# Kernel optimization log

Measured on AMD Instinct MI355X. Metric: run time of the kernel, lower is better.

## Reference

```python
import jax, jax.numpy as jnp
import numpy as np

DIM = 1024
NUM_HEADS = 16
NUM_KV_HEADS = 4
HEAD_DIM = DIM // NUM_HEADS  # 64
QK_GAIN = 1.5
ROPE_BASE = 10000.0


def _rms_norm(x, eps):
    # F.rms_norm with no weight: x / sqrt(mean(x^2) + eps)
    ms = jnp.mean(jnp.square(x), axis=-1, keepdims=True)
    return x * jax.lax.rsqrt(ms + eps)


def _rope_tables(seqlen, dim, dtype):
    inv_freq = 1.0 / (ROPE_BASE ** (jnp.arange(0, dim, 2, dtype=jnp.float32) / dim))
    freqs = jnp.outer(jnp.arange(seqlen, dtype=jnp.float32), inv_freq)  # [N, D/2]
    emb = jnp.concatenate([freqs, freqs], axis=-1)  # [N, D]
    return jnp.cos(emb).astype(dtype), jnp.sin(emb).astype(dtype)


def _apply_rope(x, cos, sin):
    # x: [B, N, H, D]; cos/sin: [N, D] broadcast over batch and heads
    half = x.shape[-1] // 2
    rot = jnp.concatenate([-x[..., half:], x[..., :half]], axis=-1)
    return x * cos[None, :, None, :] + rot * sin[None, :, None, :]


def setup_inputs() -> dict:
    key = jax.random.key(0)
    ks = jax.random.split(key, 5)
    B, N, C = 4, 2048, DIM
    s = 0.02
    return {
        "x": jax.random.normal(ks[0], (B, N, C), dtype=jnp.float32),
        "wq": jax.random.normal(ks[1], (C, C), dtype=jnp.float32) * s,
        "wk": jax.random.normal(ks[2], (C, NUM_KV_HEADS * HEAD_DIM), dtype=jnp.float32) * s,
        "wv": jax.random.normal(ks[3], (C, NUM_KV_HEADS * HEAD_DIM), dtype=jnp.float32) * s,
        "wo": jax.random.normal(ks[4], (C, C), dtype=jnp.float32) * s,
    }


def reference(x, wq, wk, wv, wo) -> jnp.ndarray:
    B, N, C = x.shape
    H, Hkv, D = NUM_HEADS, NUM_KV_HEADS, HEAD_DIM
    eps = jnp.finfo(x.dtype).eps

    q = (x @ wq).reshape(B, N, H, D)
    k = (x @ wk).reshape(B, N, Hkv, D)
    v = (x @ wv).reshape(B, N, Hkv, D)

    q = _rms_norm(q, eps)
    k = _rms_norm(k, eps)

    cos, sin = _rope_tables(N, D, q.dtype)
    q = _apply_rope(q, cos, sin) * QK_GAIN
    k = _apply_rope(k, cos, sin)

    # GQA head expansion (repeat_interleave along head dim)
    g = H // Hkv
    k = jnp.repeat(k, g, axis=2)  # [B, N, H, D]
    v = jnp.repeat(v, g, axis=2)

    # causal SDPA, scale = 1/sqrt(D)
    scores = jnp.einsum("bqhd,bkhd->bhqk", q, k) / jnp.sqrt(jnp.asarray(D, q.dtype))
    causal = jnp.tril(jnp.ones((N, N), dtype=bool))
    scores = jnp.where(causal[None, None], scores, jnp.finfo(scores.dtype).min)
    probs = jax.nn.softmax(scores, axis=-1)
    y = jnp.einsum("bhqk,bkhd->bqhd", probs, v).reshape(B, N, C)
    return y @ wo
```

## Files before the change

### kernel.cpp

```cpp
#include <hip/hip_runtime.h>

typedef __bf16 bf16;
typedef __bf16 bf16x8 __attribute__((ext_vector_type(8)));
typedef __bf16 bf16x4 __attribute__((ext_vector_type(4)));
typedef float f32x4 __attribute__((ext_vector_type(4)));

#define B_ 4
#define N_ 2048
#define C_ 1024
#define H_ 16
#define HKV_ 4
#define D_ 64

#define QSCALE 0.2705053201666806f
#define NEGINF (-1.0e30f)
#define ROPE_C (-0.41524101186092029f)

__global__ __launch_bounds__(256) void prep_qkv(const float* __restrict__ wq,
                                                const float* __restrict__ wk,
                                                const float* __restrict__ wv,
                                                bf16* __restrict__ wT) {
  __shared__ __align__(16) bf16 lds[64 * 72];
  int bx = blockIdx.x;
  const float* w;
  int ncols, tk, tn, nbase;
  if (bx < 256) {
    w = wq; ncols = 1024; tk = bx >> 4; tn = bx & 15; nbase = 0;
  } else if (bx < 320) {
    int t = bx - 256;
    w = wk; ncols = 256; tk = t >> 2; tn = t & 3; nbase = 1024;
  } else {
    int t = bx - 320;
    w = wv; ncols = 256; tk = t >> 2; tn = t & 3; nbase = 1280;
  }
  int tid = threadIdx.x;
#pragma unroll
  for (int i = 0; i < 4; ++i) {
    int c = tid + i * 256;
    int kr = c >> 4, n4 = (c & 15) * 4;
    f32x4 v = *(const f32x4*)(w + (size_t)(tk * 64 + kr) * ncols + tn * 64 + n4);
    bf16x4 b;
#pragma unroll
    for (int j = 0; j < 4; ++j) b[j] = (bf16)v[j];
    *(bf16x4*)(lds + kr * 72 + n4) = b;
  }
  __syncthreads();
#pragma unroll
  for (int i = 0; i < 2; ++i) {
    int c = tid + i * 256;
    int n = c >> 3, koff = (c & 7) * 8;
    bf16x8 tv;
#pragma unroll
    for (int j = 0; j < 8; ++j) tv[j] = lds[(koff + j) * 72 + n];
    *(bf16x8*)(wT + (size_t)(nbase + tn * 64 + n) * 1024 + tk * 64 + koff) = tv;
  }
}

__global__ __launch_bounds__(256) void prep_wo(const float* __restrict__ w,
                                               bf16* __restrict__ wT) {
  __shared__ __align__(16) bf16 lds[64 * 72];
  int tk = blockIdx.x >> 4, tn = blockIdx.x & 15;
  int tid = threadIdx.x;
#pragma unroll
  for (int i = 0; i < 4; ++i) {
    int c = tid + i * 256;
    int kr = c >> 4, n4 = (c & 15) * 4;
    f32x4 v = *(const f32x4*)(w + (size_t)(tk * 64 + kr) * 1024 + tn * 64 + n4);
    bf16x4 b;
#pragma unroll
    for (int j = 0; j < 4; ++j) b[j] = (bf16)v[j];
    *(bf16x4*)(lds + kr * 72 + n4) = b;
  }
  __syncthreads();
#pragma unroll
  for (int i = 0; i < 2; ++i) {
    int c = tid + i * 256;
    int n = c >> 3, koff = (c & 7) * 8;
    bf16x8 tv;
#pragma unroll
    for (int j = 0; j < 8; ++j) tv[j] = lds[(koff + j) * 72 + n];
    *(bf16x8*)(wT + (size_t)(tn * 64 + n) * 1024 + tk * 64 + koff) = tv;
  }
}

__global__ __launch_bounds__(256) void gemm_qkv(const float* __restrict__ x,
                                                const bf16* __restrict__ wT,
                                                bf16* __restrict__ qb,
                                                bf16* __restrict__ kvK,
                                                bf16* __restrict__ vt) {
  __shared__ __align__(16) bf16 As[128 * 72];
  __shared__ __align__(16) bf16 Bs[128 * 72];
  int by = blockIdx.y;
  int n0 = by * 128;
  int m0 = blockIdx.x * 128;
  int tid = threadIdx.x;
  int wave = tid >> 6, lane = tid & 63;
  int quad = lane >> 4, lr = lane & 15;
  int wr = (wave >> 1) * 64, wc = (wave & 1) * 64;
  int arow = tid >> 4, aoff = (tid & 15) * 4;
  int brow = tid >> 3, boff = (tid & 7) * 8;

  f32x4 acc[4][4];
  const f32x4 z = {0.f, 0.f, 0.f, 0.f};
#pragma unroll
  for (int i = 0; i < 4; ++i)
#pragma unroll
    for (int j = 0; j < 4; ++j) acc[i][j] = z;

  f32x4 sa[8];
  bf16x8 sb[4];
#pragma unroll
  for (int i = 0; i < 8; ++i)
    sa[i] = *(const f32x4*)(x + (size_t)(m0 + arow + i * 16) * 1024 + aoff);
#pragma unroll
  for (int i = 0; i < 4; ++i)
    sb[i] = *(const bf16x8*)(wT + (size_t)(n0 + brow + i * 32) * 1024 + boff);
#pragma unroll
  for (int i = 0; i < 8; ++i) {
    bf16x4 a16;
#pragma unroll
    for (int j = 0; j < 4; ++j) a16[j] = (bf16)sa[i][j];
    *(bf16x4*)(As + (arow + i * 16) * 72 + aoff) = a16;
  }
#pragma unroll
  for (int i = 0; i < 4; ++i) *(bf16x8*)(Bs + (brow + i * 32) * 72 + boff) = sb[i];
  asm volatile("s_waitcnt lgkmcnt(0)" ::: "memory");
  __builtin_amdgcn_s_barrier();
  __builtin_amdgcn_sched_barrier(0);

  for (int k0 = 0; k0 < 1024; k0 += 64) {
    bool pf = (k0 + 64 < 1024);
    if (pf) {
#pragma unroll
      for (int i = 0; i < 8; ++i)
        sa[i] = *(const f32x4*)(x + (size_t)(m0 + arow + i * 16) * 1024 + k0 + 64 + aoff);
#pragma unroll
      for (int i = 0; i < 4; ++i)
        sb[i] = *(const bf16x8*)(wT + (size_t)(n0 + brow + i * 32) * 1024 + k0 + 64 + boff);
    }
#pragma unroll
    for (int kx = 0; kx < 2; ++kx) {
      bf16x8 af[4], bfr[4];
#pragma unroll
      for (int t = 0; t < 4; ++t) {
        af[t] = *(const bf16x8*)(As + (wr + t * 16 + lr) * 72 + kx * 32 + quad * 8);
        bfr[t] = *(const bf16x8*)(Bs + (wc + t * 16 + lr) * 72 + kx * 32 + quad * 8);
      }
      __builtin_amdgcn_s_setprio(1);
#pragma unroll
      for (int rt = 0; rt < 4; ++rt)
#pragma unroll
        for (int ct = 0; ct < 4; ++ct)
          acc[rt][ct] = __builtin_amdgcn_mfma_f32_16x16x32_bf16(af[rt], bfr[ct],
                                                                acc[rt][ct], 0, 0, 0);
      __builtin_amdgcn_s_setprio(0);
    }
    __builtin_amdgcn_s_barrier();
    __builtin_amdgcn_sched_barrier(0);
    if (pf) {
#pragma unroll
      for (int i = 0; i < 8; ++i) {
        bf16x4 a16;
#pragma unroll
        for (int j = 0; j < 4; ++j) a16[j] = (bf16)sa[i][j];
        *(bf16x4*)(As + (arow + i * 16) * 72 + aoff) = a16;
      }
#pragma unroll
      for (int i = 0; i < 4; ++i) *(bf16x8*)(Bs + (brow + i * 32) * 72 + boff) = sb[i];
      asm volatile("s_waitcnt lgkmcnt(0)" ::: "memory");
    }
    __builtin_amdgcn_s_barrier();
    __builtin_amdgcn_sched_barrier(0);
  }

  if (by < 10) {
    bf16* Out;
    int ostride, ocol0;
    float oscale;
    if (by < 8) {
      Out = qb; ostride = 1024; ocol0 = by * 128; oscale = QSCALE;
    } else {
      Out = kvK; ostride = 256; ocol0 = (by - 8) * 128; oscale = 1.0f;
    }
    float if0 = exp2f(ROPE_C * (float)lr);
    float if1 = exp2f(ROPE_C * (float)(16 + lr));
#pragma unroll
    for (int rt = 0; rt < 4; ++rt) {
#pragma unroll
      for (int r = 0; r < 4; ++r) {
        float ss = 0.f;
#pragma unroll
        for (int ct = 0; ct < 4; ++ct) ss += acc[rt][ct][r] * acc[rt][ct][r];
        ss += __shfl_xor(ss, 1);
        ss += __shfl_xor(ss, 2);
        ss += __shfl_xor(ss, 4);
        ss += __shfl_xor(ss, 8);
        float rn = rsqrtf(ss * (1.0f / 64.0f) + 1.1920929e-07f);
        int row = m0 + wr + rt * 16 + quad * 4 + r;
        float fn = (float)(row & (N_ - 1));
        float sv0, cv0, sv1, cv1;
        __sincosf(fn * if0, &sv0, &cv0);
        __sincosf(fn * if1, &sv1, &cv1);
#pragma unroll
        for (int ct = 0; ct < 4; ++ct) {
          float xn = acc[rt][ct][r] * rn;
          float xp = acc[rt][ct ^ 2][r] * rn;
          float rot = (ct < 2) ? -xp : xp;
          float sv = (ct & 1) ? sv1 : sv0;
          float cv = (ct & 1) ? cv1 : cv0;
          int col = ocol0 + wc + ct * 16 + lr;
          Out[(size_t)row * ostride + col] = (bf16)((xn * cv + rot * sv) * oscale);
        }
      }
    }
  } else {
    int b = m0 >> 11;
    int tokb = (m0 & (N_ - 1)) + wr;
    int hv = (by - 10) * 2 + (wc >> 6);
#pragma unroll
    for (int rt = 0; rt < 4; ++rt)
#pragma unroll
      for (int ct = 0; ct < 4; ++ct) {
        bf16x4 ov;
#pragma unroll
        for (int r = 0; r < 4; ++r) ov[r] = (bf16)acc[rt][ct][r];
        int d = ct * 16 + lr;
        int tok = tokb + rt * 16 + quad * 4;
        *(bf16x4*)(vt + ((size_t)((b * 4 + hv) * 64 + d)) * N_ + tok) = ov;
      }
  }
}

__global__ __launch_bounds__(256) void gemm_out(const bf16* __restrict__ A,
                                                const bf16* __restrict__ Bt,
                                                float* __restrict__ C) {
  __shared__ __align__(16) bf16 As[128 * 72];
  __shared__ __align__(16) bf16 Bs[128 * 72];
  int m0 = blockIdx.x * 128, n0 = blockIdx.y * 128;
  int tid = threadIdx.x;
  int wave = tid >> 6, lane = tid & 63;
  int quad = lane >> 4, lr = lane & 15;
  int wr = (wave >> 1) * 64, wc = (wave & 1) * 64;
  int brow = tid >> 3, boff = (tid & 7) * 8;

  f32x4 acc[4][4];
  const f32x4 z = {0.f, 0.f, 0.f, 0.f};
#pragma unroll
  for (int i = 0; i < 4; ++i)
#pragma unroll
    for (int j = 0; j < 4; ++j) acc[i][j] = z;

  bf16x8 sa[4], sb[4];
#pragma unroll
  for (int i = 0; i < 4; ++i) {
    sa[i] = *(const bf16x8*)(A + (size_t)(m0 + brow + i * 32) * 1024 + boff);
    sb[i] = *(const bf16x8*)(Bt + (size_t)(n0 + brow + i * 32) * 1024 + boff);
  }
#pragma unroll
  for (int i = 0; i < 4; ++i) {
    *(bf16x8*)(As + (brow + i * 32) * 72 + boff) = sa[i];
    *(bf16x8*)(Bs + (brow + i * 32) * 72 + boff) = sb[i];
  }
  asm volatile("s_waitcnt lgkmcnt(0)" ::: "memory");
  __builtin_amdgcn_s_barrier();
  __builtin_amdgcn_sched_barrier(0);

  for (int k0 = 0; k0 < 1024; k0 += 64) {
    bool pf = (k0 + 64 < 1024);
    if (pf) {
#pragma unroll
      for (int i = 0; i < 4; ++i) {
        sa[i] = *(const bf16x8*)(A + (size_t)(m0 + brow + i * 32) * 1024 + k0 + 64 + boff);
        sb[i] = *(const bf16x8*)(Bt + (size_t)(n0 + brow + i * 32) * 1024 + k0 + 64 + boff);
      }
    }
#pragma unroll
    for (int kx = 0; kx < 2; ++kx) {
      bf16x8 af[4], bfr[4];
#pragma unroll
      for (int t = 0; t < 4; ++t) {
        af[t] = *(const bf16x8*)(As + (wr + t * 16 + lr) * 72 + kx * 32 + quad * 8);
        bfr[t] = *(const bf16x8*)(Bs + (wc + t * 16 + lr) * 72 + kx * 32 + quad * 8);
      }
      __builtin_amdgcn_s_setprio(1);
#pragma unroll
      for (int rt = 0; rt < 4; ++rt)
#pragma unroll
        for (int ct = 0; ct < 4; ++ct)
          acc[rt][ct] = __builtin_amdgcn_mfma_f32_16x16x32_bf16(af[rt], bfr[ct],
                                                                acc[rt][ct], 0, 0, 0);
      __builtin_amdgcn_s_setprio(0);
    }
    __builtin_amdgcn_s_barrier();
    __builtin_amdgcn_sched_barrier(0);
    if (pf) {
#pragma unroll
      for (int i = 0; i < 4; ++i) {
        *(bf16x8*)(As + (brow + i * 32) * 72 + boff) = sa[i];
        *(bf16x8*)(Bs + (brow + i * 32) * 72 + boff) = sb[i];
      }
      asm volatile("s_waitcnt lgkmcnt(0)" ::: "memory");
    }
    __builtin_amdgcn_s_barrier();
    __builtin_amdgcn_sched_barrier(0);
  }
#pragma unroll
  for (int rt = 0; rt < 4; ++rt)
#pragma unroll
    for (int ct = 0; ct < 4; ++ct)
#pragma unroll
      for (int r = 0; r < 4; ++r) {
        int row = m0 + wr + rt * 16 + quad * 4 + r;
        int col = n0 + wc + ct * 16 + lr;
        C[(size_t)row * 1024 + col] = acc[rt][ct][r];
      }
}

__global__ __launch_bounds__(256) void attn(bf16* __restrict__ q,
                                            const bf16* __restrict__ kv,
                                            const bf16* __restrict__ vt) {
  __shared__ __align__(16) bf16 Ks[2][64 * 64];
  __shared__ __align__(16) bf16 Vs[2][64 * 64];
  __shared__ __align__(16) bf16 Ps[64 * 64];
  int bid = blockIdx.x;
  int orig = (bid & 7) * 128 + (bid >> 3);
  int grp = orig >> 6;
  int inner = orig & 63;
  int b = grp >> 2, hkv = grp & 3;
  int h = hkv * 4 + (inner & 3);
  int p = inner >> 2;
  int tid = threadIdx.x;
  int wave = tid >> 6, lane = tid & 63;
  int quad = lane >> 4, lr = lane & 15;
  int srow = tid >> 3, soff = (tid & 7) * 8;
  int su = ((tid & 7) ^ (srow & 7)) * 8;
  int e7 = lr & 7;
  const f32x4 z = {0.f, 0.f, 0.f, 0.f};

#pragma unroll 1
  for (int s = 0; s < 2; ++s) {
    int j = s ? (31 - p) : p;
    __syncthreads();
    int qrow0 = j * 64 + wave * 16;
    int nkt = j + 1;

    bf16x8 qf[2];
#pragma unroll
    for (int kx = 0; kx < 2; ++kx)
      qf[kx] = *(const bf16x8*)(
          q + ((size_t)(b * N_ + qrow0 + lr) * H_ + h) * D_ + kx * 32 + quad * 8);

    f32x4 acc[4];
    float l_i = 0.f;
#pragma unroll
    for (int dt = 0; dt < 4; ++dt) acc[dt] = z;

    const bf16* kp = kv + (size_t)(b * N_ + srow) * 256 + hkv * 64 + soff;
    const bf16* vp = vt + ((size_t)(b * HKV_ + hkv) * 64 + srow) * N_ + soff;

    bf16x8 sk0, sk1, sv0, sv1;
    sk0 = *(const bf16x8*)(kp);
    sk1 = *(const bf16x8*)(kp + 32 * 256);
    sv0 = *(const bf16x8*)(vp);
    sv1 = *(const bf16x8*)(vp + 32 * N_);
    *(bf16x8*)(Ks[0] + srow * 64 + su) = sk0;
    *(bf16x8*)(Ks[0] + (srow + 32) * 64 + su) = sk1;
    *(bf16x8*)(Vs[0] + srow * 64 + su) = sv0;
    *(bf16x8*)(Vs[0] + (srow + 32) * 64 + su) = sv1;
    if (nkt > 1) {
      kp += 64 * 256;
      vp += 64;
      sk0 = *(const bf16x8*)(kp);
      sk1 = *(const bf16x8*)(kp + 32 * 256);
      sv0 = *(const bf16x8*)(vp);
      sv1 = *(const bf16x8*)(vp + 32 * N_);
    }
    asm volatile("s_waitcnt lgkmcnt(0)" ::: "memory");
    __builtin_amdgcn_s_barrier();
    __builtin_amdgcn_sched_barrier(0);

    int cur = 0;
    for (int kt = 0; kt < nkt; ++kt) {
      const bf16* Kc = Ks[cur];
      const bf16* Vc = Vs[cur];
      f32x4 st[4];
#pragma unroll
      for (int ct = 0; ct < 4; ++ct) st[ct] = z;
#pragma unroll
      for (int kx = 0; kx < 2; ++kx) {
        bf16x8 kf[4];
#pragma unroll
        for (int ct = 0; ct < 4; ++ct)
          kf[ct] = *(const bf16x8*)(Kc + (ct * 16 + lr) * 64 + (((kx * 4 + quad) ^ e7) * 8));
        __builtin_amdgcn_s_setprio(1);
#pragma unroll
        for (int ct = 0; ct < 4; ++ct)
          st[ct] = __builtin_amdgcn_mfma_f32_16x16x32_bf16(kf[ct], qf[kx], st[ct], 0, 0, 0);
        __builtin_amdgcn_s_setprio(0);
      }
      if (kt == j) {
        int qrow = qrow0 + lr;
#pragma unroll
        for (int ct = 0; ct < 4; ++ct)
#pragma unroll
          for (int r = 0; r < 4; ++r) {
            int key = kt * 64 + ct * 16 + quad * 4 + r;
            if (key > qrow) st[ct][r] = NEGINF;
          }
      }
      float rs = 0.f;
#pragma unroll
      for (int ct = 0; ct < 4; ++ct)
#pragma unroll
        for (int r = 0; r < 4; ++r) {
          float pv = exp2f(st[ct][r]);
          st[ct][r] = pv;
          rs += pv;
        }
      rs += __shfl_xor(rs, 16);
      rs += __shfl_xor(rs, 32);
      l_i += rs;
#pragma unroll
      for (int ct = 0; ct < 4; ++ct) {
        bf16x4 pk;
#pragma unroll
        for (int r = 0; r < 4; ++r) pk[r] = (bf16)st[ct][r];
        int pu = (((ct * 2) + (quad >> 1)) ^ e7) * 8 + (quad & 1) * 4;
        *(bf16x4*)(Ps + (wave * 16 + lr) * 64 + pu) = pk;
      }
      asm volatile("s_waitcnt lgkmcnt(0)" ::: "memory");
#pragma unroll
      for (int kx = 0; kx < 2; ++kx) {
        bf16x8 vf[4], pfr;
#pragma unroll
        for (int dt = 0; dt < 4; ++dt)
          vf[dt] = *(const bf16x8*)(Vc + (dt * 16 + lr) * 64 + (((kx * 4 + quad) ^ e7) * 8));
        pfr = *(const bf16x8*)(Ps + (wave * 16 + lr) * 64 + (((kx * 4 + quad) ^ e7) * 8));
        __builtin_amdgcn_s_setprio(1);
#pragma unroll
        for (int dt = 0; dt < 4; ++dt)
          acc[dt] = __builtin_amdgcn_mfma_f32_16x16x32_bf16(vf[dt], pfr, acc[dt], 0, 0, 0);
        __builtin_amdgcn_s_setprio(0);
      }

      bool pf = (kt + 1 < nkt);
      if (pf) {
        bf16* Kn = Ks[cur ^ 1];
        bf16* Vn = Vs[cur ^ 1];
        *(bf16x8*)(Kn + srow * 64 + su) = sk0;
        *(bf16x8*)(Kn + (srow + 32) * 64 + su) = sk1;
        *(bf16x8*)(Vn + srow * 64 + su) = sv0;
        *(bf16x8*)(Vn + (srow + 32) * 64 + su) = sv1;
        if (kt + 2 < nkt) {
          kp += 64 * 256;
          vp += 64;
          sk0 = *(const bf16x8*)(kp);
          sk1 = *(const bf16x8*)(kp + 32 * 256);
          sv0 = *(const bf16x8*)(vp);
          sv1 = *(const bf16x8*)(vp + 32 * N_);
        }
        asm volatile("s_waitcnt lgkmcnt(0)" ::: "memory");
      }
      __builtin_amdgcn_s_barrier();
      __builtin_amdgcn_sched_barrier(0);
      cur ^= 1;
    }

    float inv = 1.0f / l_i;
    int qrow = qrow0 + lr;
#pragma unroll
    for (int dt = 0; dt < 4; ++dt) {
      bf16x4 ov;
#pragma unroll
      for (int r = 0; r < 4; ++r) ov[r] = (bf16)(acc[dt][r] * inv);
      *(bf16x4*)(q + ((size_t)(b * N_ + qrow) * H_ + h) * D_ + dt * 16 + quad * 4) = ov;
    }
  }
}

extern "C" void kernel_launch(void* const* d_in, const int* in_sizes, int n_in,
                              void* d_out, int out_size, void* d_ws, size_t ws_size,
                              hipStream_t stream) {
  const float* x = (const float*)d_in[0];
  const float* wq = (const float*)d_in[1];
  const float* wk = (const float*)d_in[2];
  const float* wv = (const float*)d_in[3];
  const float* wo = (const float*)d_in[4];
  float* out = (float*)d_out;
  char* ws = (char*)d_ws;
  bf16* q = (bf16*)(ws);
  bf16* kvK = (bf16*)(ws + 16777216);
  bf16* vt = (bf16*)(ws + 20971520);
  bf16* wqkvT = (bf16*)(ws + 25165824);
  bf16* woT = (bf16*)(ws + 25165824);

  prep_qkv<<<dim3(384), 256, 0, stream>>>(wq, wk, wv, wqkvT);
  gemm_qkv<<<dim3(64, 12), 256, 0, stream>>>(x, wqkvT, q, kvK, vt);
  attn<<<dim3(1024), 256, 0, stream>>>(q, kvK, vt);
  prep_wo<<<dim3(256), 256, 0, stream>>>(wo, woT);
  gemm_out<<<dim3(64, 8), 256, 0, stream>>>(q, woT, out);
}
```

Before: 234.3 us.

## Stage GEMM tiles via direct global-to-LDS loads with XOR swizzle, pre-convert x

Adds a prep kernel that converts x to bf16, writing it into the output buffer as scratch. Both GEMMs now load tiles with global_load_lds straight into an XOR-swizzled, unpadded LDS layout instead of staging through registers. This removes the register prefetch and the manual LDS stores, but it also drops the overlap of next-tile loads with the MFMAs, so each k-step now waits at a barrier for its own loads. The extra conversion pass adds a read of x and a write of its bf16 copy.

```diff
diff --git a/kernel.cpp b/kernel.cpp
--- a/kernel.cpp
+++ b/kernel.cpp
@@ -15,6 +15,26 @@
 #define QSCALE 0.2705053201666806f
 #define NEGINF (-1.0e30f)
 #define ROPE_C (-0.41524101186092029f)
+
+__device__ __forceinline__ void glds16(const bf16* g, bf16* l) {
+  __builtin_amdgcn_global_load_lds(
+      (const __attribute__((address_space(1))) void*)g,
+      (__attribute__((address_space(3))) void*)l, 16, 0, 0);
+}
+
+__global__ __launch_bounds__(256) void prep_x(const float* __restrict__ x,
+                                              bf16* __restrict__ xb) {
+  size_t i = ((size_t)blockIdx.x * 256 + threadIdx.x) * 8;
+  f32x4 a = *(const f32x4*)(x + i);
+  f32x4 b = *(const f32x4*)(x + i + 4);
+  bf16x8 o;
+#pragma unroll
+  for (int j = 0; j < 4; ++j) {
+    o[j] = (bf16)a[j];
+    o[4 + j] = (bf16)b[j];
+  }
+  *(bf16x8*)(xb + i) = o;
+}
 
 __global__ __launch_bounds__(256) void prep_qkv(const float* __restrict__ wq,
                                                 const float* __restrict__ wk,
@@ -83,22 +103,25 @@
   }
 }
 
-__global__ __launch_bounds__(256) void gemm_qkv(const float* __restrict__ x,
+__global__ __launch_bounds__(256) void gemm_qkv(const bf16* __restrict__ xb,
                                                 const bf16* __restrict__ wT,
                                                 bf16* __restrict__ qb,
                                                 bf16* __restrict__ kvK,
                                                 bf16* __restrict__ vt) {
-  __shared__ __align__(16) bf16 As[128 * 72];
-  __shared__ __align__(16) bf16 Bs[128 * 72];
+  __shared__ __align__(16) bf16 As[128 * 64];
+  __shared__ __align__(16) bf16 Bs[128 * 64];
   int by = blockIdx.y;
   int n0 = by * 128;
   int m0 = blockIdx.x * 128;
   int tid = threadIdx.x;
-  int wave = tid >> 6, lane = tid & 63;
+  int lane = tid & 63;
+  int w8 = __builtin_amdgcn_readfirstlane(tid >> 6) * 8;
+  int wave = tid >> 6;
   int quad = lane >> 4, lr = lane & 15;
   int wr = (wave >> 1) * 64, wc = (wave & 1) * 64;
-  int arow = tid >> 4, aoff = (tid & 15) * 4;
-  int brow = tid >> 3, boff = (tid & 7) * 8;
+  int e7 = lr & 7;
+  int srow = w8 + (lane >> 3);
+  int sunit = (lane & 7) ^ (lane >> 3);
 
   f32x4 acc[4][4];
   const f32x4 z = {0.f, 0.f, 0.f, 0.f};
@@ -107,44 +130,23 @@
 #pragma unroll
     for (int j = 0; j < 4; ++j) acc[i][j] = z;
 
-  f32x4 sa[8];
-  bf16x8 sb[4];
-#pragma unroll
-  for (int i = 0; i < 8; ++i)
-    sa[i] = *(const f32x4*)(x + (size_t)(m0 + arow + i * 16) * 1024 + aoff);
-#pragma unroll
-  for (int i = 0; i < 4; ++i)
-    sb[i] = *(const bf16x8*)(wT + (size_t)(n0 + brow + i * 32) * 1024 + boff);
-#pragma unroll
-  for (int i = 0; i < 8; ++i) {
-    bf16x4 a16;
-#pragma unroll
-    for (int j = 0; j < 4; ++j) a16[j] = (bf16)sa[i][j];
-    *(bf16x4*)(As + (arow + i * 16) * 72 + aoff) = a16;
-  }
-#pragma unroll
-  for (int i = 0; i < 4; ++i) *(bf16x8*)(Bs + (brow + i * 32) * 72 + boff) = sb[i];
-  asm volatile("s_waitcnt lgkmcnt(0)" ::: "memory");
-  __builtin_amdgcn_s_barrier();
-  __builtin_amdgcn_sched_barrier(0);
-
   for (int k0 = 0; k0 < 1024; k0 += 64) {
-    bool pf = (k0 + 64 < 1024);
-    if (pf) {
-#pragma unroll
-      for (int i = 0; i < 8; ++i)
-        sa[i] = *(const f32x4*)(x + (size_t)(m0 + arow + i * 16) * 1024 + k0 + 64 + aoff);
-#pragma unroll
-      for (int i = 0; i < 4; ++i)
-        sb[i] = *(const bf16x8*)(wT + (size_t)(n0 + brow + i * 32) * 1024 + k0 + 64 + boff);
-    }
+    __syncthreads();
+#pragma unroll
+    for (int i = 0; i < 4; ++i) {
+      glds16(xb + (size_t)(m0 + i * 32 + srow) * 1024 + k0 + sunit * 8,
+             As + (i * 32 + w8) * 64);
+      glds16(wT + (size_t)(n0 + i * 32 + srow) * 1024 + k0 + sunit * 8,
+             Bs + (i * 32 + w8) * 64);
+    }
+    __syncthreads();
 #pragma unroll
     for (int kx = 0; kx < 2; ++kx) {
       bf16x8 af[4], bfr[4];
 #pragma unroll
       for (int t = 0; t < 4; ++t) {
-        af[t] = *(const bf16x8*)(As + (wr + t * 16 + lr) * 72 + kx * 32 + quad * 8);
-        bfr[t] = *(const bf16x8*)(Bs + (wc + t * 16 + lr) * 72 + kx * 32 + quad * 8);
+        af[t] = *(const bf16x8*)(As + (wr + t * 16 + lr) * 64 + (((kx * 4 + quad) ^ e7) * 8));
+        bfr[t] = *(const bf16x8*)(Bs + (wc + t * 16 + lr) * 64 + (((kx * 4 + quad) ^ e7) * 8));
       }
       __builtin_amdgcn_s_setprio(1);
 #pragma unroll
@@ -155,22 +157,6 @@
                                                                 acc[rt][ct], 0, 0, 0);
       __builtin_amdgcn_s_setprio(0);
     }
-    __builtin_amdgcn_s_barrier();
-    __builtin_amdgcn_sched_barrier(0);
-    if (pf) {
-#pragma unroll
-      for (int i = 0; i < 8; ++i) {
-        bf16x4 a16;
-#pragma unroll
-        for (int j = 0; j < 4; ++j) a16[j] = (bf16)sa[i][j];
-        *(bf16x4*)(As + (arow + i * 16) * 72 + aoff) = a16;
-      }
-#pragma unroll
-      for (int i = 0; i < 4; ++i) *(bf16x8*)(Bs + (brow + i * 32) * 72 + boff) = sb[i];
-      asm volatile("s_waitcnt lgkmcnt(0)" ::: "memory");
-    }
-    __builtin_amdgcn_s_barrier();
-    __builtin_amdgcn_sched_barrier(0);
   }
 
   if (by < 10) {
@@ -234,14 +220,18 @@
 __global__ __launch_bounds__(256) void gemm_out(const bf16* __restrict__ A,
                                                 const bf16* __restrict__ Bt,
                                                 float* __restrict__ C) {
-  __shared__ __align__(16) bf16 As[128 * 72];
-  __shared__ __align__(16) bf16 Bs[128 * 72];
+  __shared__ __align__(16) bf16 As[128 * 64];
+  __shared__ __align__(16) bf16 Bs[128 * 64];
   int m0 = blockIdx.x * 128, n0 = blockIdx.y * 128;
   int tid = threadIdx.x;
-  int wave = tid >> 6, lane = tid & 63;
+  int lane = tid & 63;
+  int w8 = __builtin_amdgcn_readfirstlane(tid >> 6) * 8;
+  int wave = tid >> 6;
   int quad = lane >> 4, lr = lane & 15;
   int wr = (wave >> 1) * 64, wc = (wave & 1) * 64;
-  int brow = tid >> 3, boff = (tid & 7) * 8;
+  int e7 = lr & 7;
+  int srow = w8 + (lane >> 3);
+  int sunit = (lane & 7) ^ (lane >> 3);
 
   f32x4 acc[4][4];
   const f32x4 z = {0.f, 0.f, 0.f, 0.f};
@@ -250,37 +240,23 @@
 #pragma unroll
     for (int j = 0; j < 4; ++j) acc[i][j] = z;
 
-  bf16x8 sa[4], sb[4];
-#pragma unroll
-  for (int i = 0; i < 4; ++i) {
-    sa[i] = *(const bf16x8*)(A + (size_t)(m0 + brow + i * 32) * 1024 + boff);
-    sb[i] = *(const bf16x8*)(Bt + (size_t)(n0 + brow + i * 32) * 1024 + boff);
-  }
-#pragma unroll
-  for (int i = 0; i < 4; ++i) {
-    *(bf16x8*)(As + (brow + i * 32) * 72 + boff) = sa[i];
-    *(bf16x8*)(Bs + (brow + i * 32) * 72 + boff) = sb[i];
-  }
-  asm volatile("s_waitcnt lgkmcnt(0)" ::: "memory");
-  __builtin_amdgcn_s_barrier();
-  __builtin_amdgcn_sched_barrier(0);
-
   for (int k0 = 0; k0 < 1024; k0 += 64) {
-    bool pf = (k0 + 64 < 1024);
-    if (pf) {
-#pragma unroll
-      for (int i = 0; i < 4; ++i) {
-        sa[i] = *(const bf16x8*)(A + (size_t)(m0 + brow + i * 32) * 1024 + k0 + 64 + boff);
-        sb[i] = *(const bf16x8*)(Bt + (size_t)(n0 + brow + i * 32) * 1024 + k0 + 64 + boff);
-      }
-    }
+    __syncthreads();
+#pragma unroll
+    for (int i = 0; i < 4; ++i) {
+      glds16(A + (size_t)(m0 + i * 32 + srow) * 1024 + k0 + sunit * 8,
+             As + (i * 32 + w8) * 64);
+      glds16(Bt + (size_t)(n0 + i * 32 + srow) * 1024 + k0 + sunit * 8,
+             Bs + (i * 32 + w8) * 64);
+    }
+    __syncthreads();
 #pragma unroll
     for (int kx = 0; kx < 2; ++kx) {
       bf16x8 af[4], bfr[4];
 #pragma unroll
       for (int t = 0; t < 4; ++t) {
-        af[t] = *(const bf16x8*)(As + (wr + t * 16 + lr) * 72 + kx * 32 + quad * 8);
-        bfr[t] = *(const bf16x8*)(Bs + (wc + t * 16 + lr) * 72 + kx * 32 + quad * 8);
+        af[t] = *(const bf16x8*)(As + (wr + t * 16 + lr) * 64 + (((kx * 4 + quad) ^ e7) * 8));
+        bfr[t] = *(const bf16x8*)(Bs + (wc + t * 16 + lr) * 64 + (((kx * 4 + quad) ^ e7) * 8));
       }
       __builtin_amdgcn_s_setprio(1);
 #pragma unroll
@@ -291,18 +267,6 @@
                                                                 acc[rt][ct], 0, 0, 0);
       __builtin_amdgcn_s_setprio(0);
     }
-    __builtin_amdgcn_s_barrier();
-    __builtin_amdgcn_sched_barrier(0);
-    if (pf) {
-#pragma unroll
-      for (int i = 0; i < 4; ++i) {
-        *(bf16x8*)(As + (brow + i * 32) * 72 + boff) = sa[i];
-        *(bf16x8*)(Bs + (brow + i * 32) * 72 + boff) = sb[i];
-      }
-      asm volatile("s_waitcnt lgkmcnt(0)" ::: "memory");
-    }
-    __builtin_amdgcn_s_barrier();
-    __builtin_amdgcn_sched_barrier(0);
   }
 #pragma unroll
   for (int rt = 0; rt < 4; ++rt)
@@ -493,9 +457,11 @@
   bf16* vt = (bf16*)(ws + 20971520);
   bf16* wqkvT = (bf16*)(ws + 25165824);
   bf16* woT = (bf16*)(ws + 25165824);
-
+  bf16* xb = (bf16*)d_out;
+
+  prep_x<<<dim3(4096), 256, 0, stream>>>(x, xb);
   prep_qkv<<<dim3(384), 256, 0, stream>>>(wq, wk, wv, wqkvT);
-  gemm_qkv<<<dim3(64, 12), 256, 0, stream>>>(x, wqkvT, q, kvK, vt);
+  gemm_qkv<<<dim3(64, 12), 256, 0, stream>>>(xb, wqkvT, q, kvK, vt);
   attn<<<dim3(1024), 256, 0, stream>>>(q, kvK, vt);
   prep_wo<<<dim3(256), 256, 0, stream>>>(wo, woT);
   gemm_out<<<dim3(64, 8), 256, 0, stream>>>(q, woT, out);
```

Result: no change. 235.4 us (+0.5%).
